# Kernel optimization log

Measured on AMD Instinct MI355X. Metric: run time of the kernel, lower is better.

## Reference

```python
import jax, jax.numpy as jnp
import numpy as np


def setup_inputs() -> dict:
    key = jax.random.key(0)
    kH, kU, kW = jax.random.split(key, 3)
    T, J, D2 = 16384, 1024, 512  # T x 2d context, J x 2d query
    H = jax.random.normal(kH, (T, D2), dtype=jnp.float32)
    U = jax.random.normal(kU, (J, D2), dtype=jnp.float32)
    Ws = jax.random.normal(kW, (3 * D2, 1), dtype=jnp.float32) * 0.05
    return {"H": H, "U": U, "Ws": Ws}


def reference(H, U, Ws):
    D2 = H.shape[-1]
    # Ws applied to concat([H_dup, U_dup, H_dup*U_dup]) decomposes into three blocks.
    w1 = Ws[:D2, 0]          # (2d,)
    w2 = Ws[D2:2 * D2, 0]    # (2d,)
    w3 = Ws[2 * D2:, 0]      # (2d,)
    # Trilinear similarity S[t, j] = H[t]@w1 + U[j]@w2 + (H[t]*U[j])@w3  -> (T, J)
    S = (H @ w1)[:, None] + (U @ w2)[None, :] + (H * w3) @ U.T
    # C2Q attention: softmax over query axis, attend query vectors -> (T, 2d)
    attended_query = jax.nn.softmax(S, axis=-1) @ U
    # Q2C attention: softmax over T of max_j S, rank-1 summary of context -> (2d,)
    b = jax.nn.softmax(jnp.max(S, axis=-1))
    h_tilde = b @ H  # (2d,), tiled to (T, 2d) by broadcasting
    # Merge to query-aware representation G -> (T, 8d)
    G = jnp.concatenate(
        [H, attended_query, H * attended_query, H * h_tilde[None, :]], axis=-1
    )
    return G
```

## Files before the change

kernel.cpp:

```cpp
#include <hip/hip_runtime.h>
#include <hip/hip_bf16.h>

#define T_ROWS 16384
#define J_DIM  1024
#define D_DIM  512

typedef __attribute__((ext_vector_type(8))) short bf16x8;
typedef __attribute__((ext_vector_type(4))) float f32x4;
typedef unsigned short u16;

__device__ __forceinline__ u16 f2bf(float f) {
    union { float f; unsigned int u; } v; v.f = f;
    return (u16)((v.u + 0x7FFFu + ((v.u >> 16) & 1u)) >> 16);
}

__device__ __forceinline__ void gload16(const void* g, void* l) {
    __builtin_amdgcn_global_load_lds(
        (__attribute__((address_space(1))) void*)(unsigned long long)(size_t)g,
        (__attribute__((address_space(3))) void*)(unsigned int)(size_t)l,
        16, 0, 0);
}

template<int NT>
__device__ __forceinline__ void gemm_core(
    const u16* A, int lda, const u16* B, int ldb, u16* lds, f32x4 (&acc)[4][4])
{
    const int tid  = threadIdx.x;
    const int lane = tid & 63;
    const int w    = tid >> 6;
    const int wr   = w >> 1, wc = w & 1;
    const int fr   = lane & 15, quad = lane >> 4;

    const int srow = tid >> 2;
    const int ss   = (tid & 3) ^ ((srow >> 1) & 3);

    const u16* gA0 = A + (size_t)srow * lda + ss * 8;
    const u16* gA1 = A + (size_t)(srow + 64) * lda + ss * 8;
    const u16* gB0 = B + (size_t)srow * ldb + ss * 8;
    const u16* gB1 = B + (size_t)(srow + 64) * ldb + ss * 8;

    u16* As = lds;
    u16* Bs = lds + 8192;
    u16* dA0 = As + tid * 8;
    u16* dA1 = As + 2048 + tid * 8;
    u16* dB0 = Bs + tid * 8;
    u16* dB1 = Bs + 2048 + tid * 8;

    gload16(gA0, dA0); gload16(gA1, dA1);
    gload16(gB0, dB0); gload16(gB1, dB1);
    gA0 += 32; gA1 += 32; gB0 += 32; gB1 += 32;

    int offA[4], offB[4];
    #pragma unroll
    for (int i = 0; i < 4; ++i) {
        const int rA = wr * 64 + i * 16 + fr;
        offA[i] = rA * 32 + (quad ^ ((rA >> 1) & 3)) * 8;
        const int rB = wc * 64 + i * 16 + fr;
        offB[i] = rB * 32 + (quad ^ ((rB >> 1) & 3)) * 8;
    }
    __syncthreads();

    #pragma unroll 2
    for (int t = 0; t < NT; ++t) {
        const int cur = (t & 1) * 4096;
        const int nxt = 4096 - cur;
        if (t + 1 < NT) {
            gload16(gA0, dA0 + nxt); gload16(gA1, dA1 + nxt);
            gload16(gB0, dB0 + nxt); gload16(gB1, dB1 + nxt);
            gA0 += 32; gA1 += 32; gB0 += 32; gB1 += 32;
        }
        const u16* Ac = As + cur;
        const u16* Bc = Bs + cur;
        bf16x8 af[4], bfr[4];
        #pragma unroll
        for (int i = 0; i < 4; ++i) af[i]  = *(const bf16x8*)(Ac + offA[i]);
        #pragma unroll
        for (int i = 0; i < 4; ++i) bfr[i] = *(const bf16x8*)(Bc + offB[i]);
        #pragma unroll
        for (int mf = 0; mf < 4; ++mf)
            #pragma unroll
            for (int nf = 0; nf < 4; ++nf)
                acc[mf][nf] = __builtin_amdgcn_mfma_f32_16x16x32_bf16(
                    af[mf], bfr[nf], acc[mf][nf], 0, 0, 0);
        __syncthreads();
    }
}

__global__ __launch_bounds__(128) void prep_u(
    const float* __restrict__ U, const float* __restrict__ Ws,
    float* __restrict__ uw2, u16* __restrict__ Ub, u16* __restrict__ Ut)
{
    const int j = blockIdx.x;
    const int t = threadIdx.x;
    const float4 u  = ((const float4*)(U + (size_t)j * D_DIM))[t];
    const float4 w2 = ((const float4*)(Ws + D_DIM))[t];
    float p = u.x * w2.x + u.y * w2.y + u.z * w2.z + u.w * w2.w;
    #pragma unroll
    for (int m = 1; m < 64; m <<= 1) p += __shfl_xor(p, m);
    __shared__ float red[2];
    if ((t & 63) == 0) red[t >> 6] = p;
    __syncthreads();
    if (t == 0) uw2[j] = red[0] + red[1];

    ushort4 v;
    v.x = f2bf(u.x); v.y = f2bf(u.y); v.z = f2bf(u.z); v.w = f2bf(u.w);
    ((ushort4*)(Ub + (size_t)j * D_DIM))[t] = v;
    const u16 bs[4] = { v.x, v.y, v.z, v.w };
    #pragma unroll
    for (int s = 0; s < 4; ++s)
        Ut[(size_t)(4 * t + s) * J_DIM + j] = bs[s];
}

__global__ __launch_bounds__(128) void prep_h(
    const float* __restrict__ H, const float* __restrict__ Ws,
    float* __restrict__ hw1, u16* outU)
{
    const int i = blockIdx.x;
    const int t = threadIdx.x;
    const float4 h  = ((const float4*)(H + (size_t)i * D_DIM))[t];
    const float4 w1 = ((const float4*)Ws)[t];
    const float4 w3 = ((const float4*)(Ws + 2 * D_DIM))[t];
    float p = h.x * w1.x + h.y * w1.y + h.z * w1.z + h.w * w1.w;
    #pragma unroll
    for (int m = 1; m < 64; m <<= 1) p += __shfl_xor(p, m);
    __shared__ float red[2];
    if ((t & 63) == 0) red[t >> 6] = p;
    __syncthreads();
    if (t == 0) hw1[i] = red[0] + red[1];

    ushort4 q;
    q.x = f2bf(h.x * w3.x); q.y = f2bf(h.y * w3.y);
    q.z = f2bf(h.z * w3.z); q.w = f2bf(h.w * w3.w);
    *(ushort4*)(outU + (size_t)i * 4096 + 3072 + 4 * t) = q;
}

__global__ __launch_bounds__(256) void s_gemm(
    u16* outU, const u16* __restrict__ Ub, const float* __restrict__ uw2)
{
    __shared__ u16 lds[16384];
    const int bid = blockIdx.x;
    const int swz = (bid & 7) * 128 + (bid >> 3);
    const int bm = swz >> 3, nb = swz & 7;

    f32x4 acc[4][4];
    #pragma unroll
    for (int i = 0; i < 4; ++i)
        #pragma unroll
        for (int j = 0; j < 4; ++j) acc[i][j] = (f32x4){0.f, 0.f, 0.f, 0.f};

    gemm_core<16>(outU + (size_t)bm * 128 * 4096 + 3072, 4096,
                  Ub + (size_t)nb * 128 * 512, 512, lds, acc);

    const int tid = threadIdx.x, lane = tid & 63, w = tid >> 6;
    const int wr = w >> 1, wc = w & 1, fr = lane & 15, quad = lane >> 4;
    float* outF = (float*)outU;
    int jc[4]; float u2[4];
    #pragma unroll
    for (int nf = 0; nf < 4; ++nf) {
        jc[nf] = nb * 128 + wc * 64 + nf * 16 + fr;
        u2[nf] = uw2[jc[nf]];
    }
    #pragma unroll
    for (int mf = 0; mf < 4; ++mf)
        #pragma unroll
        for (int m = 0; m < 4; ++m) {
            const size_t row = bm * 128 + wr * 64 + mf * 16 + quad * 4 + m;
            float* rp = outF + row * 2048;
            #pragma unroll
            for (int nf = 0; nf < 4; ++nf) rp[jc[nf]] = acc[mf][nf][m] + u2[nf];
        }
}

__global__ __launch_bounds__(256) void softmax_kernel(
    u16* outU, const float* __restrict__ hw1, float* __restrict__ rstat)
{
    const int lane = threadIdx.x & 63;
    const int w = threadIdx.x >> 6;
    const size_t row = (size_t)blockIdx.x * 4 + w;
    float* outF = (float*)outU;
    float4 v[4];
    #pragma unroll
    for (int e = 0; e < 4; ++e)
        v[e] = *(const float4*)(outF + row * 2048 + e * 256 + lane * 4);
    float mx = -1e30f;
    #pragma unroll
    for (int e = 0; e < 4; ++e)
        mx = fmaxf(mx, fmaxf(fmaxf(v[e].x, v[e].y), fmaxf(v[e].z, v[e].w)));
    #pragma unroll
    for (int s = 1; s < 64; s <<= 1) mx = fmaxf(mx, __shfl_xor(mx, s));
    float sum = 0.f;
    #pragma unroll
    for (int e = 0; e < 4; ++e) {
        v[e].x = __expf(v[e].x - mx); v[e].y = __expf(v[e].y - mx);
        v[e].z = __expf(v[e].z - mx); v[e].w = __expf(v[e].w - mx);
        sum += v[e].x + v[e].y + v[e].z + v[e].w;
    }
    #pragma unroll
    for (int s = 1; s < 64; s <<= 1) sum += __shfl_xor(sum, s);
    const float inv = 1.f / sum;
    #pragma unroll
    for (int e = 0; e < 4; ++e) {
        ushort4 p;
        p.x = f2bf(v[e].x * inv); p.y = f2bf(v[e].y * inv);
        p.z = f2bf(v[e].z * inv); p.w = f2bf(v[e].w * inv);
        *(ushort4*)(outU + row * 4096 + 1024 + e * 256 + lane * 4) = p;
    }
    if (lane == 0) rstat[row] = mx + hw1[row];
}

__global__ __launch_bounds__(1024) void bsoft_kernel(
    const float* __restrict__ r, float* __restrict__ b)
{
    __shared__ float red[16];
    __shared__ float Msh, Lsh;
    const int t = threadIdx.x;
    float m = -1e30f;
    #pragma unroll
    for (int e = 0; e < 16; ++e) m = fmaxf(m, r[t + e * 1024]);
    #pragma unroll
    for (int s = 1; s < 64; s <<= 1) m = fmaxf(m, __shfl_xor(m, s));
    if ((t & 63) == 0) red[t >> 6] = m;
    __syncthreads();
    if (t == 0) {
        float M = red[0];
        for (int i = 1; i < 16; ++i) M = fmaxf(M, red[i]);
        Msh = M;
    }
    __syncthreads();
    const float M = Msh;
    float l = 0.f;
    #pragma unroll
    for (int e = 0; e < 16; ++e) l += __expf(r[t + e * 1024] - M);
    #pragma unroll
    for (int s = 1; s < 64; s <<= 1) l += __shfl_xor(l, s);
    if ((t & 63) == 0) red[t >> 6] = l;
    __syncthreads();
    if (t == 0) {
        float L = 0.f;
        for (int i = 0; i < 16; ++i) L += red[i];
        Lsh = L;
    }
    __syncthreads();
    const float invL = 1.f / Lsh;
    #pragma unroll
    for (int e = 0; e < 16; ++e) b[t + e * 1024] = __expf(r[t + e * 1024] - M) * invL;
}

__global__ __launch_bounds__(512) void htilde_partial(
    const float* __restrict__ H, const float* __restrict__ b,
    float* __restrict__ part)
{
    const int blk = blockIdx.x;
    const int d = threadIdx.x;
    const int i0 = blk * 64;
    float s = 0.f;
    for (int rI = 0; rI < 64; ++rI)
        s += b[i0 + rI] * H[(size_t)(i0 + rI) * D_DIM + d];
    part[(size_t)blk * D_DIM + d] = s;
}

__global__ __launch_bounds__(512) void htilde_reduce(
    const float* __restrict__ part, float* __restrict__ ht)
{
    const int d = threadIdx.x;
    float s = 0.f;
    for (int p = 0; p < 256; ++p) s += part[(size_t)p * D_DIM + d];
    ht[d] = s;
}

__global__ __launch_bounds__(256) void pv_gemm(
    u16* outU, const u16* __restrict__ Ut, const float* __restrict__ H,
    const float* __restrict__ htld)
{
    __shared__ u16 lds[16384];
    const int bid = blockIdx.x;
    const int swz = (bid & 7) * 64 + (bid >> 3);
    const int bm = swz >> 2, nb = swz & 3;

    f32x4 acc[4][4];
    #pragma unroll
    for (int i = 0; i < 4; ++i)
        #pragma unroll
        for (int j = 0; j < 4; ++j) acc[i][j] = (f32x4){0.f, 0.f, 0.f, 0.f};

    gemm_core<32>(outU + (size_t)bm * 128 * 4096 + 1024, 4096,
                  Ut + (size_t)nb * 128 * 1024, 1024, lds, acc);

    const int tid = threadIdx.x, lane = tid & 63, w = tid >> 6;
    const int wr = w >> 1, wc = w & 1, fr = lane & 15, quad = lane >> 4;
    float* outF = (float*)outU;
    int c[4]; float ht[4];
    #pragma unroll
    for (int nf = 0; nf < 4; ++nf) {
        c[nf] = nb * 128 + wc * 64 + nf * 16 + fr;
        ht[nf] = htld[c[nf]];
    }
    #pragma unroll
    for (int mf = 0; mf < 4; ++mf)
        #pragma unroll
        for (int m = 0; m < 4; ++m) {
            const size_t row = bm * 128 + wr * 64 + mf * 16 + quad * 4 + m;
            const float* hrow = H + row * D_DIM;
            float* ob = outF + row * 2048;
            #pragma unroll
            for (int nf = 0; nf < 4; ++nf) {
                const float h  = hrow[c[nf]];
                const float aq = acc[mf][nf][m];
                ob[c[nf]]        = h;
                ob[512 + c[nf]]  = aq;
                ob[1024 + c[nf]] = h * aq;
                ob[1536 + c[nf]] = h * ht[nf];
            }
        }
}

extern "C" void kernel_launch(void* const* d_in, const int* in_sizes, int n_in,
                              void* d_out, int out_size, void* d_ws, size_t ws_size,
                              hipStream_t stream)
{
    const float* H  = (const float*)d_in[0];
    const float* U  = (const float*)d_in[1];
    const float* Ws = (const float*)d_in[2];
    u16* outU = (u16*)d_out;

    float* uw2   = (float*)d_ws;
    float* rstat = uw2 + 1024;
    float* bvec  = rstat + T_ROWS;
    float* hw1   = bvec + T_ROWS;
    float* htld  = hw1 + T_ROWS;
    float* part  = htld + D_DIM;
    u16*   Ub    = (u16*)(part + 256 * D_DIM);
    u16*   Ut    = Ub + (size_t)J_DIM * D_DIM;

    hipLaunchKernelGGL(prep_u, dim3(J_DIM), dim3(128), 0, stream, U, Ws, uw2, Ub, Ut);
    hipLaunchKernelGGL(prep_h, dim3(T_ROWS), dim3(128), 0, stream, H, Ws, hw1, outU);
    hipLaunchKernelGGL(s_gemm, dim3(1024), dim3(256), 0, stream, outU, Ub, uw2);
    hipLaunchKernelGGL(softmax_kernel, dim3(T_ROWS / 4), dim3(256), 0, stream,
                       outU, hw1, rstat);
    hipLaunchKernelGGL(bsoft_kernel, dim3(1), dim3(1024), 0, stream, rstat, bvec);
    hipLaunchKernelGGL(htilde_partial, dim3(256), dim3(512), 0, stream, H, bvec, part);
    hipLaunchKernelGGL(htilde_reduce, dim3(1), dim3(512), 0, stream, part, htld);
    hipLaunchKernelGGL(pv_gemm, dim3(512), dim3(256), 0, stream, outU, Ut, H, htld);
}
```

Measured before the change: 132.1 us.

## Fuse row softmax into PV GEMM and compute row maxima in S GEMM epilogue

Result: no change. 130.8 us (-1.0%).

```diff
diff --git a/kernel.cpp b/kernel.cpp
--- a/kernel.cpp
+++ b/kernel.cpp
@@ -12,6 +12,10 @@
 __device__ __forceinline__ u16 f2bf(float f) {
     union { float f; unsigned int u; } v; v.f = f;
     return (u16)((v.u + 0x7FFFu + ((v.u >> 16) & 1u)) >> 16);
+}
+__device__ __forceinline__ float bf2f(u16 b) {
+    union { unsigned int u; float f; } v; v.u = ((unsigned int)b) << 16;
+    return v.f;
 }
 
 __device__ __forceinline__ void gload16(const void* g, void* l) {
@@ -88,7 +92,7 @@
 
 __global__ __launch_bounds__(128) void prep_u(
     const float* __restrict__ U, const float* __restrict__ Ws,
-    float* __restrict__ uw2, u16* __restrict__ Ub, u16* __restrict__ Ut)
+    float* __restrict__ uw2, u16* __restrict__ Ub, u16* __restrict__ Utp)
 {
     const int j = blockIdx.x;
     const int t = threadIdx.x;
@@ -105,10 +109,14 @@
     ushort4 v;
     v.x = f2bf(u.x); v.y = f2bf(u.y); v.z = f2bf(u.z); v.w = f2bf(u.w);
     ((ushort4*)(Ub + (size_t)j * D_DIM))[t] = v;
+
+    const size_t jpart = (size_t)(j >> 5) * 512 + (size_t)(((j >> 3) & 3) * 128) + (j & 7);
     const u16 bs[4] = { v.x, v.y, v.z, v.w };
     #pragma unroll
-    for (int s = 0; s < 4; ++s)
-        Ut[(size_t)(4 * t + s) * J_DIM + j] = bs[s];
+    for (int s = 0; s < 4; ++s) {
+        const int d = 4 * t + s;
+        Utp[(size_t)(d >> 4) * 16384 + jpart + (size_t)(d & 15) * 8] = bs[s];
+    }
 }
 
 __global__ __launch_bounds__(128) void prep_h(
@@ -135,7 +143,8 @@
 }
 
 __global__ __launch_bounds__(256) void s_gemm(
-    u16* outU, const u16* __restrict__ Ub, const float* __restrict__ uw2)
+    u16* outU, const u16* __restrict__ Ub, const float* __restrict__ uw2,
+    float* __restrict__ pmax)
 {
     __shared__ u16 lds[16384];
     const int bid = blockIdx.x;
@@ -153,70 +162,70 @@
 
     const int tid = threadIdx.x, lane = tid & 63, w = tid >> 6;
     const int wr = w >> 1, wc = w & 1, fr = lane & 15, quad = lane >> 4;
-    float* outF = (float*)outU;
     int jc[4]; float u2[4];
     #pragma unroll
     for (int nf = 0; nf < 4; ++nf) {
         jc[nf] = nb * 128 + wc * 64 + nf * 16 + fr;
         u2[nf] = uw2[jc[nf]];
     }
+    float* redf = (float*)lds;
     #pragma unroll
     for (int mf = 0; mf < 4; ++mf)
         #pragma unroll
         for (int m = 0; m < 4; ++m) {
-            const size_t row = bm * 128 + wr * 64 + mf * 16 + quad * 4 + m;
-            float* rp = outF + row * 2048;
-            #pragma unroll
-            for (int nf = 0; nf < 4; ++nf) rp[jc[nf]] = acc[mf][nf][m] + u2[nf];
-        }
-}
-
-__global__ __launch_bounds__(256) void softmax_kernel(
-    u16* outU, const float* __restrict__ hw1, float* __restrict__ rstat)
-{
-    const int lane = threadIdx.x & 63;
-    const int w = threadIdx.x >> 6;
-    const size_t row = (size_t)blockIdx.x * 4 + w;
-    float* outF = (float*)outU;
-    float4 v[4];
-    #pragma unroll
-    for (int e = 0; e < 4; ++e)
-        v[e] = *(const float4*)(outF + row * 2048 + e * 256 + lane * 4);
-    float mx = -1e30f;
-    #pragma unroll
-    for (int e = 0; e < 4; ++e)
-        mx = fmaxf(mx, fmaxf(fmaxf(v[e].x, v[e].y), fmaxf(v[e].z, v[e].w)));
-    #pragma unroll
-    for (int s = 1; s < 64; s <<= 1) mx = fmaxf(mx, __shfl_xor(mx, s));
-    float sum = 0.f;
-    #pragma unroll
-    for (int e = 0; e < 4; ++e) {
-        v[e].x = __expf(v[e].x - mx); v[e].y = __expf(v[e].y - mx);
-        v[e].z = __expf(v[e].z - mx); v[e].w = __expf(v[e].w - mx);
-        sum += v[e].x + v[e].y + v[e].z + v[e].w;
-    }
-    #pragma unroll
-    for (int s = 1; s < 64; s <<= 1) sum += __shfl_xor(sum, s);
-    const float inv = 1.f / sum;
-    #pragma unroll
-    for (int e = 0; e < 4; ++e) {
-        ushort4 p;
-        p.x = f2bf(v[e].x * inv); p.y = f2bf(v[e].y * inv);
-        p.z = f2bf(v[e].z * inv); p.w = f2bf(v[e].w * inv);
-        *(ushort4*)(outU + row * 4096 + 1024 + e * 256 + lane * 4) = p;
-    }
-    if (lane == 0) rstat[row] = mx + hw1[row];
-}
-
-__global__ __launch_bounds__(1024) void bsoft_kernel(
-    const float* __restrict__ r, float* __restrict__ b)
+            float mv = -1e30f;
+            #pragma unroll
+            for (int nf = 0; nf < 4; ++nf) {
+                acc[mf][nf][m] += u2[nf];
+                mv = fmaxf(mv, acc[mf][nf][m]);
+            }
+            mv = fmaxf(mv, __shfl_xor(mv, 1));
+            mv = fmaxf(mv, __shfl_xor(mv, 2));
+            mv = fmaxf(mv, __shfl_xor(mv, 4));
+            mv = fmaxf(mv, __shfl_xor(mv, 8));
+            if (fr == 0) redf[wc * 128 + wr * 64 + mf * 16 + quad * 4 + m] = mv;
+        }
+    __syncthreads();
+    if (wc == 0 && fr == 0) {
+        #pragma unroll
+        for (int mf = 0; mf < 4; ++mf)
+            #pragma unroll
+            for (int m = 0; m < 4; ++m) {
+                const int rr = wr * 64 + mf * 16 + quad * 4 + m;
+                pmax[((size_t)bm * 128 + rr) * 8 + nb] =
+                    fmaxf(redf[rr], redf[128 + rr]);
+            }
+    }
+    #pragma unroll
+    for (int mf = 0; mf < 4; ++mf)
+        #pragma unroll
+        for (int m = 0; m < 4; ++m) {
+            const size_t row = (size_t)bm * 128 + wr * 64 + mf * 16 + quad * 4 + m;
+            u16* rp = outU + row * 4096 + 1024;
+            #pragma unroll
+            for (int nf = 0; nf < 4; ++nf) rp[jc[nf]] = f2bf(acc[mf][nf][m]);
+        }
+}
+
+__global__ __launch_bounds__(1024) void bsoft2(
+    const float* __restrict__ pmax, const float* __restrict__ hw1,
+    float* __restrict__ bvec)
 {
     __shared__ float red[16];
     __shared__ float Msh, Lsh;
     const int t = threadIdx.x;
+    float rs[16];
+    #pragma unroll
+    for (int e = 0; e < 16; ++e) {
+        const int r = t + e * 1024;
+        const float4 p0 = *(const float4*)(pmax + (size_t)r * 8);
+        const float4 p1 = *(const float4*)(pmax + (size_t)r * 8 + 4);
+        rs[e] = fmaxf(fmaxf(fmaxf(p0.x, p0.y), fmaxf(p0.z, p0.w)),
+                      fmaxf(fmaxf(p1.x, p1.y), fmaxf(p1.z, p1.w))) + hw1[r];
+    }
     float m = -1e30f;
     #pragma unroll
-    for (int e = 0; e < 16; ++e) m = fmaxf(m, r[t + e * 1024]);
+    for (int e = 0; e < 16; ++e) m = fmaxf(m, rs[e]);
     #pragma unroll
     for (int s = 1; s < 64; s <<= 1) m = fmaxf(m, __shfl_xor(m, s));
     if ((t & 63) == 0) red[t >> 6] = m;
@@ -230,7 +239,7 @@
     const float M = Msh;
     float l = 0.f;
     #pragma unroll
-    for (int e = 0; e < 16; ++e) l += __expf(r[t + e * 1024] - M);
+    for (int e = 0; e < 16; ++e) l += __expf(rs[e] - M);
     #pragma unroll
     for (int s = 1; s < 64; s <<= 1) l += __shfl_xor(l, s);
     if ((t & 63) == 0) red[t >> 6] = l;
@@ -243,7 +252,7 @@
     __syncthreads();
     const float invL = 1.f / Lsh;
     #pragma unroll
-    for (int e = 0; e < 16; ++e) b[t + e * 1024] = __expf(r[t + e * 1024] - M) * invL;
+    for (int e = 0; e < 16; ++e) bvec[t + e * 1024] = __expf(rs[e] - M) * invL;
 }
 
 __global__ __launch_bounds__(512) void htilde_partial(
@@ -268,14 +277,63 @@
     ht[d] = s;
 }
 
-__global__ __launch_bounds__(256) void pv_gemm(
-    u16* outU, const u16* __restrict__ Ut, const float* __restrict__ H,
+__global__ __launch_bounds__(512) void pv_fused(
+    u16* outU, const u16* __restrict__ Utp, const float* __restrict__ H,
     const float* __restrict__ htld)
 {
-    __shared__ u16 lds[16384];
-    const int bid = blockIdx.x;
-    const int swz = (bid & 7) * 64 + (bid >> 3);
-    const int bm = swz >> 2, nb = swz & 3;
+    __shared__ u16 SP[64 * 1024];
+    const int tid = threadIdx.x, lane = tid & 63, w = tid >> 6;
+    const int fr = lane & 15, quad = lane >> 4;
+    const int ib = blockIdx.x * 64;
+
+    {
+        const int r_off = tid >> 7;
+        const int c8 = tid & 127;
+        #pragma unroll
+        for (int p = 0; p < 16; ++p) {
+            const int r = p * 4 + r_off;
+            gload16(outU + (size_t)(ib + r) * 4096 + 1024 + (size_t)((c8 ^ (r & 7)) * 8),
+                    SP + (size_t)p * 4096 + (size_t)tid * 8);
+        }
+    }
+    __syncthreads();
+
+    #pragma unroll
+    for (int rr = 0; rr < 8; ++rr) {
+        const int r = w * 8 + rr;
+        u16* row = SP + (size_t)r * 1024;
+        const int s0 = (lane ^ rr) * 8;
+        const int s1 = ((lane + 64) ^ rr) * 8;
+        bf16x8 x0 = *(bf16x8*)(row + s0);
+        bf16x8 x1 = *(bf16x8*)(row + s1);
+        float f0[8], f1[8];
+        float mx = -1e30f;
+        #pragma unroll
+        for (int i = 0; i < 8; ++i) {
+            f0[i] = bf2f((u16)x0[i]); f1[i] = bf2f((u16)x1[i]);
+            mx = fmaxf(mx, fmaxf(f0[i], f1[i]));
+        }
+        #pragma unroll
+        for (int s = 1; s < 64; s <<= 1) mx = fmaxf(mx, __shfl_xor(mx, s));
+        float sum = 0.f;
+        #pragma unroll
+        for (int i = 0; i < 8; ++i) {
+            f0[i] = __expf(f0[i] - mx); f1[i] = __expf(f1[i] - mx);
+            sum += f0[i] + f1[i];
+        }
+        #pragma unroll
+        for (int s = 1; s < 64; s <<= 1) sum += __shfl_xor(sum, s);
+        const float inv = 1.f / sum;
+        bf16x8 y0, y1;
+        #pragma unroll
+        for (int i = 0; i < 8; ++i) {
+            y0[i] = (short)f2bf(f0[i] * inv);
+            y1[i] = (short)f2bf(f1[i] * inv);
+        }
+        *(bf16x8*)(row + s0) = y0;
+        *(bf16x8*)(row + s1) = y1;
+    }
+    __syncthreads();
 
     f32x4 acc[4][4];
     #pragma unroll
@@ -283,33 +341,64 @@
         #pragma unroll
         for (int j = 0; j < 4; ++j) acc[i][j] = (f32x4){0.f, 0.f, 0.f, 0.f};
 
-    gemm_core<32>(outU + (size_t)bm * 128 * 4096 + 1024, 4096,
-                  Ut + (size_t)nb * 128 * 1024, 1024, lds, acc);
-
-    const int tid = threadIdx.x, lane = tid & 63, w = tid >> 6;
-    const int wr = w >> 1, wc = w & 1, fr = lane & 15, quad = lane >> 4;
-    float* outF = (float*)outU;
-    int c[4]; float ht[4];
-    #pragma unroll
-    for (int nf = 0; nf < 4; ++nf) {
-        c[nf] = nb * 128 + wc * 64 + nf * 16 + fr;
-        ht[nf] = htld[c[nf]];
-    }
+    const u16* bp = Utp + (size_t)lane * 8;
+    bf16x8 bA[4], bB[4];
+    #pragma unroll
+    for (int nf = 0; nf < 4; ++nf)
+        bA[nf] = *(const bf16x8*)(bp + ((size_t)(w * 4 + nf) * 32) * 512);
+
+    for (int ks = 0; ks < 32; ks += 2) {
+        #pragma unroll
+        for (int nf = 0; nf < 4; ++nf)
+            bB[nf] = *(const bf16x8*)(bp + ((size_t)(w * 4 + nf) * 32 + ks + 1) * 512);
+        bf16x8 a0[4];
+        #pragma unroll
+        for (int mf = 0; mf < 4; ++mf)
+            a0[mf] = *(const bf16x8*)(SP + (size_t)(mf * 16 + fr) * 1024
+                                         + (size_t)(((ks * 4 + quad) ^ (fr & 7)) * 8));
+        #pragma unroll
+        for (int mf = 0; mf < 4; ++mf)
+            #pragma unroll
+            for (int nf = 0; nf < 4; ++nf)
+                acc[mf][nf] = __builtin_amdgcn_mfma_f32_16x16x32_bf16(
+                    a0[mf], bA[nf], acc[mf][nf], 0, 0, 0);
+        if (ks + 2 < 32) {
+            #pragma unroll
+            for (int nf = 0; nf < 4; ++nf)
+                bA[nf] = *(const bf16x8*)(bp + ((size_t)(w * 4 + nf) * 32 + ks + 2) * 512);
+        }
+        bf16x8 a1[4];
+        #pragma unroll
+        for (int mf = 0; mf < 4; ++mf)
+            a1[mf] = *(const bf16x8*)(SP + (size_t)(mf * 16 + fr) * 1024
+                                         + (size_t)((((ks + 1) * 4 + quad) ^ (fr & 7)) * 8));
+        #pragma unroll
+        for (int mf = 0; mf < 4; ++mf)
+            #pragma unroll
+            for (int nf = 0; nf < 4; ++nf)
+                acc[mf][nf] = __builtin_amdgcn_mfma_f32_16x16x32_bf16(
+                    a1[mf], bB[nf], acc[mf][nf], 0, 0, 0);
+    }
+
+    float ht[4];
+    #pragma unroll
+    for (int nf = 0; nf < 4; ++nf) ht[nf] = htld[w * 64 + nf * 16 + fr];
     #pragma unroll
     for (int mf = 0; mf < 4; ++mf)
         #pragma unroll
         for (int m = 0; m < 4; ++m) {
-            const size_t row = bm * 128 + wr * 64 + mf * 16 + quad * 4 + m;
+            const size_t row = (size_t)ib + mf * 16 + quad * 4 + m;
             const float* hrow = H + row * D_DIM;
-            float* ob = outF + row * 2048;
+            float* ob = (float*)outU + row * 2048;
             #pragma unroll
             for (int nf = 0; nf < 4; ++nf) {
-                const float h  = hrow[c[nf]];
+                const int c = w * 64 + nf * 16 + fr;
+                const float h  = hrow[c];
                 const float aq = acc[mf][nf][m];
-                ob[c[nf]]        = h;
-                ob[512 + c[nf]]  = aq;
-                ob[1024 + c[nf]] = h * aq;
-                ob[1536 + c[nf]] = h * ht[nf];
+                ob[c]        = h;
+                ob[512 + c]  = aq;
+                ob[1024 + c] = h * aq;
+                ob[1536 + c] = h * ht[nf];
             }
         }
 }
@@ -324,21 +413,20 @@
     u16* outU = (u16*)d_out;
 
     float* uw2   = (float*)d_ws;
-    float* rstat = uw2 + 1024;
-    float* bvec  = rstat + T_ROWS;
-    float* hw1   = bvec + T_ROWS;
-    float* htld  = hw1 + T_ROWS;
+    float* hw1   = uw2 + 1024;
+    float* bvec  = hw1 + T_ROWS;
+    float* htld  = bvec + T_ROWS;
     float* part  = htld + D_DIM;
-    u16*   Ub    = (u16*)(part + 256 * D_DIM);
-    u16*   Ut    = Ub + (size_t)J_DIM * D_DIM;
-
-    hipLaunchKernelGGL(prep_u, dim3(J_DIM), dim3(128), 0, stream, U, Ws, uw2, Ub, Ut);
+    float* pmax  = part + 256 * D_DIM;
+    u16*   Ub    = (u16*)(pmax + (size_t)T_ROWS * 8);
+    u16*   Utp   = Ub + (size_t)J_DIM * D_DIM;
+
+    hipLaunchKernelGGL(prep_u, dim3(J_DIM), dim3(128), 0, stream, U, Ws, uw2, Ub, Utp);
     hipLaunchKernelGGL(prep_h, dim3(T_ROWS), dim3(128), 0, stream, H, Ws, hw1, outU);
-    hipLaunchKernelGGL(s_gemm, dim3(1024), dim3(256), 0, stream, outU, Ub, uw2);
-    hipLaunchKernelGGL(softmax_kernel, dim3(T_ROWS / 4), dim3(256), 0, stream,
-                       outU, hw1, rstat);
-    hipLaunchKernelGGL(bsoft_kernel, dim3(1), dim3(1024), 0, stream, rstat, bvec);
+    hipLaunchKernelGGL(s_gemm, dim3(1024), dim3(256), 0, stream, outU, Ub, uw2, pmax);
+    hipLaunchKernelGGL(bsoft2, dim3(1), dim3(1024), 0, stream, pmax, hw1, bvec);
     hipLaunchKernelGGL(htilde_partial, dim3(256), dim3(512), 0, stream, H, bvec, part);
     hipLaunchKernelGGL(htilde_reduce, dim3(1), dim3(512), 0, stream, part, htld);
-    hipLaunchKernelGGL(pv_gemm, dim3(512), dim3(256), 0, stream, outU, Ut, H, htld);
-}
+    hipLaunchKernelGGL(pv_fused, dim3(T_ROWS / 64), dim3(512), 0, stream,
+                       outU, Utp, H, htld);
+}
```
